# Performance work log

Measured on AMD Instinct MI355X. Metric: run time of the kernel, lower is better.

Reference implementation:

```python
import jax, jax.numpy as jnp
import numpy as np

WIN = 11
SIGMA = 1.5
K1, K2 = 0.01, 0.03
DATA_RANGE = 1.0


def _gauss1d(size, sigma):
    coords = jnp.arange(size, dtype=jnp.float32) - size // 2
    g = jnp.exp(-(coords ** 2) / (2.0 * sigma ** 2))
    return g / g.sum()


def _blur(x, g):
    # Separable depthwise Gaussian blur, VALID padding, matching F.conv2d(groups=C).
    C = x.shape[1]
    w = g.astype(x.dtype)
    kh = jnp.broadcast_to(w.reshape(1, 1, WIN, 1), (C, 1, WIN, 1))  # blur along H
    kw = jnp.broadcast_to(w.reshape(1, 1, 1, WIN), (C, 1, 1, WIN))  # blur along W
    dn = ('NCHW', 'OIHW', 'NCHW')
    out = jax.lax.conv_general_dilated(x, kh, (1, 1), 'VALID',
                                       dimension_numbers=dn, feature_group_count=C)
    out = jax.lax.conv_general_dilated(out, kw, (1, 1), 'VALID',
                                       dimension_numbers=dn, feature_group_count=C)
    return out


def setup_inputs() -> dict:
    key = jax.random.key(0)
    k1, k2 = jax.random.split(key)
    shape = (16, 3, 512, 512)
    image1 = jax.random.uniform(k1, shape, dtype=jnp.float32)
    image2 = jax.random.uniform(k2, shape, dtype=jnp.float32)
    window = _gauss1d(WIN, SIGMA)
    return {"image1": image1, "image2": image2, "window": window}


def reference(image1, image2, window):
    c1 = (K1 * DATA_RANGE) ** 2
    c2 = (K2 * DATA_RANGE) ** 2
    mu1 = _blur(image1, window)
    mu2 = _blur(image2, window)
    mu1_sq = mu1 * mu1
    mu2_sq = mu2 * mu2
    mu1_mu2 = mu1 * mu2
    sigma1_sq = _blur(image1 * image1, window) - mu1_sq
    sigma2_sq = _blur(image2 * image2, window) - mu2_sq
    sigma12 = _blur(image1 * image2, window) - mu1_mu2
    cs_map = (2.0 * sigma12 + c2) / (sigma1_sq + sigma2_sq + c2)
    ssim_map = (2.0 * mu1_mu2 + c1) / (mu1_sq + mu2_sq + c1) * cs_map
    # flatten(2).mean(-1) then .mean() over (B,C) == full mean (uniform sizes)
    return ssim_map.mean()
```

## Files before the change

### kernel.cpp

```cpp
#include <hip/hip_runtime.h>

#define WIN   11
#define IW    512
#define IH    512
#define OW    502
#define OH    502
#define NCH   48
#define TW    118
#define SWC   128
#define SWP   134
#define CH    8
#define NCHUNK 4
#define SLABH (CH*NCHUNK)
#define NGX   5
#define NGY   16

typedef float v2f __attribute__((ext_vector_type(2)));

__device__ __forceinline__ float fast_rcp(float x) {
    return __builtin_amdgcn_rcpf(x);
}

template<bool EDGE>
__device__ __forceinline__ void ssim_slab(const float* __restrict__ p1,
                                          const float* __restrict__ p2,
                                          const float (&w)[WIN],
                                          v2f (*vbuf)[CH][SWP],
                                          int x0, int y0, int tid, float& acc)
{
    const int c = tid;
    int gx = x0 + c;
    if (EDGE) gx = min(gx, IW - 1);

    v2f h[10];
#pragma unroll
    for (int j = 0; j < 10; ++j) {
        int gy = y0 + j; if (EDGE) gy = min(gy, IH - 1);
        const int gidx = gy * IW + gx;
        h[j].x = p1[gidx];
        h[j].y = p2[gidx];
    }

    const int rh = tid & 7;
    const int g  = tid >> 3;
    const int xs = g * 8;
    const float c1 = 0.0001f;
    const float c2 = 0.0009f;

#pragma unroll
    for (int ci = 0; ci < NCHUNK; ++ci) {
        const int jbase = y0 + 10 + ci * CH;
        v2f n[CH];
#pragma unroll
        for (int j = 0; j < CH; ++j) {
            int gy = jbase + j; if (EDGE) gy = min(gy, IH - 1);
            const int gidx = gy * IW + gx;
            n[j].x = p1[gidx];
            n[j].y = p2[gidx];
        }

        v2f accA[CH], accB[CH];
#pragma unroll
        for (int r = 0; r < CH; ++r) {
            accA[r] = (v2f){0.f, 0.f};
            accB[r] = (v2f){0.f, 0.f};
        }
#pragma unroll
        for (int j = 0; j < CH + 10; ++j) {
            v2f ab = (j < 10) ? h[j] : n[j - 10];
            v2f st;
            st.x = fmaf(ab.x, ab.x, ab.y * ab.y);
            st.y = ab.x * ab.y;
#pragma unroll
            for (int k = 0; k < WIN; ++k) {
                const int r = j - k;
                if (r >= 0 && r < CH) {
                    v2f ws; ws.x = w[k]; ws.y = w[k];
                    accA[r] = __builtin_elementwise_fma(ws, ab, accA[r]);
                    accB[r] = __builtin_elementwise_fma(ws, st, accB[r]);
                }
            }
        }
#pragma unroll
        for (int r = 0; r < CH; ++r) {
            vbuf[0][r][c] = accA[r];
            vbuf[1][r][c] = accB[r];
        }
#pragma unroll
        for (int j = 0; j < 10; ++j)
            h[j] = (j < 2) ? h[8 + j] : n[j - 2];

        __syncthreads();

        if (g < 15) {
            v2f resA[8], resB[8];
#pragma unroll
            for (int q = 0; q < 2; ++q) {
                v2f x2[18];
                const float4* src = reinterpret_cast<const float4*>(&vbuf[q][rh][xs]);
#pragma unroll
                for (int t = 0; t < 9; ++t) {
                    float4 f = src[t];
                    x2[2*t+0].x = f.x; x2[2*t+0].y = f.y;
                    x2[2*t+1].x = f.z; x2[2*t+1].y = f.w;
                }
#pragma unroll
                for (int o = 0; o < 8; ++o) {
                    v2f s = {0.f, 0.f};
#pragma unroll
                    for (int k = 0; k < WIN; ++k) {
                        v2f ws; ws.x = w[k]; ws.y = w[k];
                        s = __builtin_elementwise_fma(ws, x2[o + k], s);
                    }
                    if (q == 0) resA[o] = s; else resB[o] = s;
                }
            }

            const int oy = y0 + ci * CH + rh;
#pragma unroll
            for (int o = 0; o < 8; ++o) {
                const int tc = xs + o;
                bool valid = (tc < TW);
                if (EDGE) valid = valid && (oy < OH) && ((x0 + tc) < OW);
                if (valid) {
                    float m1 = resA[o].x, m2 = resA[o].y;
                    float mu11 = m1 * m1, mu22 = m2 * m2, mu12 = m1 * m2;
                    float sAB = resB[o].x - mu11 - mu22;
                    float s12 = resB[o].y - mu12;
                    float num = (2.f * mu12 + c1) * (2.f * s12 + c2);
                    float den = (mu11 + mu22 + c1) * (sAB + c2);
                    acc += num * fast_rcp(den);
                }
            }
        }
        __syncthreads();
    }
}

__global__ __launch_bounds__(128, 4)
void ssim_fused_kernel(const float* __restrict__ img1,
                       const float* __restrict__ img2,
                       const float* __restrict__ win,
                       float* __restrict__ partial)
{
    __shared__ __align__(16) v2f vbuf[2][CH][SWP];
    __shared__ float wavesum[2];

    const int tid = threadIdx.x;
    const int ch = blockIdx.z;
    const int x0 = blockIdx.x * TW;
    const int y0 = blockIdx.y * SLABH;
    const float* __restrict__ p1 = img1 + (size_t)ch * (IW * IH);
    const float* __restrict__ p2 = img2 + (size_t)ch * (IW * IH);

    float w[WIN];
#pragma unroll
    for (int k = 0; k < WIN; ++k) w[k] = win[k];

    float acc = 0.f;
    const bool edge = (blockIdx.x == gridDim.x - 1) || (blockIdx.y == gridDim.y - 1);
    if (edge) ssim_slab<true >(p1, p2, w, vbuf, x0, y0, tid, acc);
    else      ssim_slab<false>(p1, p2, w, vbuf, x0, y0, tid, acc);

#pragma unroll
    for (int off = 32; off > 0; off >>= 1)
        acc += __shfl_down(acc, off, 64);
    if ((tid & 63) == 0) wavesum[tid >> 6] = acc;
    __syncthreads();
    if (tid == 0) {
        partial[(size_t)blockIdx.z * (gridDim.x * gridDim.y)
                + blockIdx.y * gridDim.x + blockIdx.x] = wavesum[0] + wavesum[1];
    }
}

__global__ __launch_bounds__(256)
void reduce_partials_kernel(const float* __restrict__ partial, int n4,
                            float* __restrict__ out, double inv_count)
{
    __shared__ double sd[256];
    const float4* p4 = reinterpret_cast<const float4*>(partial);
    double s = 0.0;
    for (int i = threadIdx.x; i < n4; i += 256) {
        float4 f = p4[i];
        s += (double)f.x + (double)f.y + (double)f.z + (double)f.w;
    }
    sd[threadIdx.x] = s;
    __syncthreads();
    for (int off = 128; off > 0; off >>= 1) {
        if (threadIdx.x < off) sd[threadIdx.x] += sd[threadIdx.x + off];
        __syncthreads();
    }
    if (threadIdx.x == 0)
        out[0] = (float)(sd[0] * inv_count);
}

extern "C" void kernel_launch(void* const* d_in, const int* in_sizes, int n_in,
                              void* d_out, int out_size, void* d_ws, size_t ws_size,
                              hipStream_t stream)
{
    const float* img1 = (const float*)d_in[0];
    const float* img2 = (const float*)d_in[1];
    const float* win  = (const float*)d_in[2];
    float* out = (float*)d_out;
    float* partial = (float*)d_ws;

    dim3 grid(NGX, NGY, NCH);
    dim3 block(128);

    ssim_fused_kernel<<<grid, block, 0, stream>>>(img1, img2, win, partial);

    const int nblocks = NGX * NGY * NCH;
    const double inv_count = 1.0 / ((double)NCH * OW * OH);
    reduce_partials_kernel<<<1, 256, 0, stream>>>(partial, nblocks / 4, out, inv_count);
}
```

Measured before the change: 49.88 us.

## Shrink column tile to one 64-thread wave with 7-pixel horizontal work

Halves the tile width to 54 output columns so each block is a single 64-lane wave. That removes the cross-wave shared-memory reduction and lets every thread do horizontal-pass work, with 7 outputs per thread instead of 8 and no idle group. Vertical results are now written to shared memory as each row finishes rather than at the end, which may shorten register live ranges. In exchange the 10-column halo overhead per tile roughly doubles relative to useful output, and the grid doubles in block count.

```diff
diff --git a/kernel.cpp b/kernel.cpp
--- a/kernel.cpp
+++ b/kernel.cpp
@@ -6,14 +6,15 @@
 #define OW    502
 #define OH    502
 #define NCH   48
-#define TW    118
-#define SWC   128
-#define SWP   134
+#define TW    54
+#define SWC   64
+#define SWP   66
 #define CH    8
 #define NCHUNK 4
 #define SLABH (CH*NCHUNK)
-#define NGX   5
+#define NGX   10
 #define NGY   16
+#define PXL   7
 
 typedef float v2f __attribute__((ext_vector_type(2)));
 
@@ -41,9 +42,9 @@
         h[j].y = p2[gidx];
     }
 
-    const int rh = tid & 7;
-    const int g  = tid >> 3;
-    const int xs = g * 8;
+    const int rh = tid >> 3;
+    const int gg = tid & 7;
+    const int xs = gg * PXL;
     const float c1 = 0.0001f;
     const float c2 = 0.0009f;
 
@@ -80,11 +81,10 @@
                     accB[r] = __builtin_elementwise_fma(ws, st, accB[r]);
                 }
             }
-        }
-#pragma unroll
-        for (int r = 0; r < CH; ++r) {
-            vbuf[0][r][c] = accA[r];
-            vbuf[1][r][c] = accB[r];
+            if (j >= 10) {
+                vbuf[0][j - 10][c] = accA[j - 10];
+                vbuf[1][j - 10][c] = accB[j - 10];
+            }
         }
 #pragma unroll
         for (int j = 0; j < 10; ++j)
@@ -92,20 +92,17 @@
 
         __syncthreads();
 
-        if (g < 15) {
-            v2f resA[8], resB[8];
+        {
+            v2f resA[PXL], resB[PXL];
 #pragma unroll
             for (int q = 0; q < 2; ++q) {
-                v2f x2[18];
-                const float4* src = reinterpret_cast<const float4*>(&vbuf[q][rh][xs]);
-#pragma unroll
-                for (int t = 0; t < 9; ++t) {
-                    float4 f = src[t];
-                    x2[2*t+0].x = f.x; x2[2*t+0].y = f.y;
-                    x2[2*t+1].x = f.z; x2[2*t+1].y = f.w;
-                }
-#pragma unroll
-                for (int o = 0; o < 8; ++o) {
+                v2f x2[PXL + 10];
+                const v2f* src = &vbuf[q][rh][xs];
+#pragma unroll
+                for (int t = 0; t < PXL + 10; ++t)
+                    x2[t] = src[t];
+#pragma unroll
+                for (int o = 0; o < PXL; ++o) {
                     v2f s = {0.f, 0.f};
 #pragma unroll
                     for (int k = 0; k < WIN; ++k) {
@@ -118,7 +115,7 @@
 
             const int oy = y0 + ci * CH + rh;
 #pragma unroll
-            for (int o = 0; o < 8; ++o) {
+            for (int o = 0; o < PXL; ++o) {
                 const int tc = xs + o;
                 bool valid = (tc < TW);
                 if (EDGE) valid = valid && (oy < OH) && ((x0 + tc) < OW);
@@ -137,15 +134,13 @@
     }
 }
 
-__global__ __launch_bounds__(128, 4)
+__global__ __launch_bounds__(64, 4)
 void ssim_fused_kernel(const float* __restrict__ img1,
                        const float* __restrict__ img2,
                        const float* __restrict__ win,
                        float* __restrict__ partial)
 {
     __shared__ __align__(16) v2f vbuf[2][CH][SWP];
-    __shared__ float wavesum[2];
-
     const int tid = threadIdx.x;
     const int ch = blockIdx.z;
     const int x0 = blockIdx.x * TW;
@@ -165,11 +160,9 @@
 #pragma unroll
     for (int off = 32; off > 0; off >>= 1)
         acc += __shfl_down(acc, off, 64);
-    if ((tid & 63) == 0) wavesum[tid >> 6] = acc;
-    __syncthreads();
     if (tid == 0) {
         partial[(size_t)blockIdx.z * (gridDim.x * gridDim.y)
-                + blockIdx.y * gridDim.x + blockIdx.x] = wavesum[0] + wavesum[1];
+                + blockIdx.y * gridDim.x + blockIdx.x] = acc;
     }
 }
 
@@ -205,7 +198,7 @@
     float* partial = (float*)d_ws;
 
     dim3 grid(NGX, NGY, NCH);
-    dim3 block(128);
+    dim3 block(64);
 
     ssim_fused_kernel<<<grid, block, 0, stream>>>(img1, img2, win, partial);
 
```

Result: faster. 47.77 us (median of 2 runs) (-4.2%).
